# Optimization experiments

Measured on AMD Instinct MI355X. Metric: run time of the kernel, lower is better.

Reference implementation:

```python
import jax, jax.numpy as jnp
import numpy as np


def setup_inputs() -> dict:
    key = jax.random.key(0)
    B, H, C, T = 8, 8, 64, 2048
    qkv = jax.random.normal(key, (B, 3 * H * C, T), dtype=jnp.float32)
    return {"qkv": qkv, "n_heads": H}


def reference(qkv, n_heads):
    # qkv: (B, 3*H*C, T)
    bs, width, length = qkv.shape
    ch = width // (3 * n_heads)
    q, k, v = jnp.split(qkv, 3, axis=1)          # each (B, H*C, T)
    scale = ch ** (-0.25)
    q = (q * scale).reshape(bs * n_heads, ch, length)
    k = (k * scale).reshape(bs * n_heads, ch, length)
    v = v.reshape(bs * n_heads, ch, length)
    # weight[b, t, s] = sum_c q[b,c,t] * k[b,c,s]
    weight = jnp.einsum('bct,bcs->bts', q, k)
    weight = jax.nn.softmax(weight.astype(jnp.float32), axis=-1).astype(qkv.dtype)
    out = jnp.einsum('bts,bcs->bct', weight, v)   # (B*H, C, T)
    return out.reshape(bs, n_heads * ch, length)
```

## Files before the change

### kernel.cpp

```cpp
#include <hip/hip_runtime.h>

typedef __bf16 bf16x4 __attribute__((ext_vector_type(4)));
typedef __bf16 bf16x8 __attribute__((ext_vector_type(8)));
typedef float floatx4 __attribute__((ext_vector_type(4)));
typedef float floatx16 __attribute__((ext_vector_type(16)));
typedef unsigned uintx2 __attribute__((ext_vector_type(2)));

#define T_SEQ 2048
#define TTILE 512
#define STILE 64
#define LOG2E_SCALE 0.18033688011112042f

__device__ __forceinline__ unsigned cvt_pk_bf16(float a, float b) {
    unsigned r;
    asm("v_cvt_pk_bf16_f32 %0, %1, %2" : "=v"(r) : "v"(a), "v"(b));
    return r;
}
__device__ __forceinline__ unsigned short bf16_bits(float a) {
    return (unsigned short)((__builtin_bit_cast(unsigned, a) + 0x8000u) >> 16);
}

__global__ __launch_bounds__(512, 2) void attn_fused(
    const float* __restrict__ qkv, float* __restrict__ out)
{
    __shared__ __align__(16) __bf16 Kt[2][STILE][72];
    __shared__ __align__(16) __bf16 Vs[2][64][72];

    const int tid  = threadIdx.x;
    const int lane = tid & 63;
    const int wave = tid >> 6;
    const int l31  = lane & 31;
    const int g    = lane >> 5;

    const int bh = blockIdx.y;
    const int b = bh >> 3, head = bh & 7;
    const size_t in_base = ((size_t)b * 1536 + head * 64) * T_SEQ;
    const float* Qg = qkv + in_base;
    const float* Kg = qkv + in_base + (size_t)512 * T_SEQ;
    const float* Vg = qkv + in_base + (size_t)1024 * T_SEQ;

    const int tcol0 = blockIdx.x * TTILE + wave * 64 + l31;
    const int tcol1 = tcol0 + 32;

    bf16x8 qf[2][4];
    #pragma unroll
    for (int kb = 0; kb < 4; ++kb)
        #pragma unroll
        for (int j = 0; j < 8; ++j) {
            size_t rowoff = (size_t)(kb * 16 + g * 8 + j) * T_SEQ;
            qf[0][kb][j] = (__bf16)(Qg[rowoff + tcol0] * LOG2E_SCALE);
            qf[1][kb][j] = (__bf16)(Qg[rowoff + tcol1] * LOG2E_SCALE);
        }

    floatx16 zf;
    #pragma unroll
    for (int r = 0; r < 16; ++r) zf[r] = 0.0f;

    union U4 { unsigned u[4]; bf16x8 v; };
    U4 one0, one1;
    {
        unsigned p0 = (l31 == 0) ? 0x3F803F80u : 0u;
        unsigned p1 = (l31 == 1) ? 0x3F803F80u : 0u;
        one0.u[0] = p0; one0.u[1] = p0; one0.u[2] = p0; one0.u[3] = p0;
        one1.u[0] = p1; one1.u[1] = p1; one1.u[2] = p1; one1.u[3] = p1;
    }

    floatx16 Oa[2][2];
    floatx16 La = zf;
    Oa[0][0] = zf; Oa[0][1] = zf; Oa[1][0] = zf; Oa[1][1] = zf;

    int cc[2], ss[2];
    size_t goff[2];
    #pragma unroll
    for (int r = 0; r < 2; ++r) {
        int i = tid + r * 512;
        cc[r] = i >> 4;
        ss[r] = (i & 15) * 4;
        goff[r] = (size_t)cc[r] * T_SEQ + ss[r];
    }
    const int ph = (tid >> 1) & 3;

    floatx4 kr[2], vr[2];
    #pragma unroll
    for (int r = 0; r < 2; ++r) {
        kr[r] = *(const floatx4*)(Kg + goff[r]);
        vr[r] = *(const floatx4*)(Vg + goff[r]);
    }
    #pragma unroll
    for (int r = 0; r < 2; ++r) {
        int c = cc[r], s4 = ss[r];
        #pragma unroll
        for (int k = 0; k < 4; ++k) {
            int d = (k + ph) & 3;
            *(unsigned short*)&Kt[0][s4 + d][c] = bf16_bits(kr[r][d]);
        }
        union { unsigned u[2]; bf16x4 v; } vb;
        vb.u[0] = cvt_pk_bf16(vr[r][0], vr[r][1]);
        vb.u[1] = cvt_pk_bf16(vr[r][2], vr[r][3]);
        *(bf16x4*)&Vs[0][c][s4] = vb.v;
    }

#define QKTSTEP(ROWB, SaT0, SaT1)                                             \
    {                                                                         \
        bf16x8 kf = *(const bf16x8*)&KtR[(ROWB) + l31][g * 8];                \
        SaT0 = __builtin_amdgcn_mfma_f32_32x32x16_bf16(kf, qf[0][0], zf, 0, 0, 0); \
        SaT1 = __builtin_amdgcn_mfma_f32_32x32x16_bf16(kf, qf[1][0], zf, 0, 0, 0); \
    }                                                                         \
    _Pragma("unroll")                                                         \
    for (int kb = 1; kb < 4; ++kb) {                                          \
        bf16x8 kf = *(const bf16x8*)&KtR[(ROWB) + l31][kb * 16 + g * 8];      \
        SaT0 = __builtin_amdgcn_mfma_f32_32x32x16_bf16(kf, qf[0][kb], SaT0, 0, 0, 0); \
        SaT1 = __builtin_amdgcn_mfma_f32_32x32x16_bf16(kf, qf[1][kb], SaT1, 0, 0, 0); \
    }

#define SOFTMAX2(SaT0, SaT1, pf)                                              \
    _Pragma("unroll")                                                         \
    for (int tt = 0; tt < 2; ++tt) {                                          \
        const floatx16& Sa_ = tt ? SaT1 : SaT0;                               \
        float p_[16];                                                         \
        _Pragma("unroll")                                                     \
        for (int r = 0; r < 16; ++r)                                          \
            p_[r] = __builtin_amdgcn_exp2f(Sa_[r]);                           \
        unsigned d_[8];                                                       \
        _Pragma("unroll")                                                     \
        for (int q = 0; q < 8; ++q)                                           \
            d_[q] = cvt_pk_bf16(p_[2 * q], p_[2 * q + 1]);                    \
        _Pragma("unroll")                                                     \
        for (int kb = 0; kb < 2; ++kb) {                                      \
            uintx2 s02 = __builtin_amdgcn_permlane32_swap(                    \
                d_[4 * kb + 0], d_[4 * kb + 2], false, false);                \
            uintx2 s13 = __builtin_amdgcn_permlane32_swap(                    \
                d_[4 * kb + 1], d_[4 * kb + 3], false, false);                \
            U4 fu_;                                                           \
            fu_.u[0] = s02[0]; fu_.u[1] = s13[0];                             \
            fu_.u[2] = s02[1]; fu_.u[3] = s13[1];                             \
            pf[tt][kb] = fu_.v;                                               \
        }                                                                     \
    }

#define PVSTEP(pf, kb2base)                                                   \
    _Pragma("unroll")                                                         \
    for (int mc = 0; mc < 2; ++mc)                                            \
        _Pragma("unroll")                                                     \
        for (int kb = 0; kb < 2; ++kb) {                                      \
            bf16x8 vf = *(const bf16x8*)&VsR[mc * 32 + l31][(kb2base + kb) * 16 + g * 8]; \
            Oa[0][mc] = __builtin_amdgcn_mfma_f32_32x32x16_bf16(vf, pf[0][kb], Oa[0][mc], 0, 0, 0); \
            Oa[1][mc] = __builtin_amdgcn_mfma_f32_32x32x16_bf16(vf, pf[1][kb], Oa[1][mc], 0, 0, 0); \
        }                                                                     \
    _Pragma("unroll")                                                         \
    for (int kb = 0; kb < 2; ++kb) {                                          \
        La = __builtin_amdgcn_mfma_f32_32x32x16_bf16(one0.v, pf[0][kb], La, 0, 0, 0); \
        La = __builtin_amdgcn_mfma_f32_32x32x16_bf16(one1.v, pf[1][kb], La, 0, 0, 0); \
    }

    for (int it = 0; it < T_SEQ / STILE; ++it) {
        const int rb = it & 1;
        const int s_next = (it + 1) * STILE;
        const bool pref = (s_next < T_SEQ);

        __syncthreads();

        if (pref) {
            #pragma unroll
            for (int r = 0; r < 2; ++r) {
                kr[r] = *(const floatx4*)(Kg + goff[r] + s_next);
                vr[r] = *(const floatx4*)(Vg + goff[r] + s_next);
            }
        }

        const __bf16 (*KtR)[72] = Kt[rb];
        const __bf16 (*VsR)[72] = Vs[rb];

        floatx16 Sa00, Sa01;
        QKTSTEP(0, Sa00, Sa01)

        bf16x8 pfA[2][2];
        SOFTMAX2(Sa00, Sa01, pfA)

        floatx16 Sa10, Sa11;
        QKTSTEP(32, Sa10, Sa11)

        PVSTEP(pfA, 0)

        bf16x8 pfB[2][2];
        SOFTMAX2(Sa10, Sa11, pfB)

        PVSTEP(pfB, 2)

        if (pref) {
            __bf16 (*KtW)[72] = Kt[rb ^ 1];
            __bf16 (*VsW)[72] = Vs[rb ^ 1];
            #pragma unroll
            for (int r = 0; r < 2; ++r) {
                int c = cc[r], s4 = ss[r];
                #pragma unroll
                for (int k = 0; k < 4; ++k) {
                    int d = (k + ph) & 3;
                    *(unsigned short*)&KtW[s4 + d][c] = bf16_bits(kr[r][d]);
                }
                union { unsigned u[2]; bf16x4 v; } vb;
                vb.u[0] = cvt_pk_bf16(vr[r][0], vr[r][1]);
                vb.u[1] = cvt_pk_bf16(vr[r][2], vr[r][3]);
                *(bf16x4*)&VsW[c][s4] = vb.v;
            }
        }
    }

    float d0 = La[0], d1 = La[1];
    float rl0 = 1.0f / (d0 + __shfl_xor(d0, 32));
    float rl1 = 1.0f / (d1 + __shfl_xor(d1, 32));

    const size_t out_base = ((size_t)b * 512 + head * 64) * T_SEQ;
    #pragma unroll
    for (int mc = 0; mc < 2; ++mc)
        #pragma unroll
        for (int r = 0; r < 16; ++r) {
            int c = mc * 32 + (r & 3) + 8 * (r >> 2) + 4 * g;
            size_t row = out_base + (size_t)c * T_SEQ;
            out[row + tcol0] = Oa[0][mc][r] * rl0;
            out[row + tcol1] = Oa[1][mc][r] * rl1;
        }
}

extern "C" void kernel_launch(void* const* d_in, const int* in_sizes, int n_in,
                              void* d_out, int out_size, void* d_ws, size_t ws_size,
                              hipStream_t stream) {
    const float* qkv = (const float*)d_in[0];
    float* out = (float*)d_out;
    dim3 grid(T_SEQ / TTILE, 64);
    attn_fused<<<grid, dim3(512), 0, stream>>>(qkv, out);
}
```

Measured before the change: 202.7 us.

## Halve per-wave query tile, raise occupancy, and remap blocks for XCD locality

```diff
diff --git a/kernel.cpp b/kernel.cpp
--- a/kernel.cpp
+++ b/kernel.cpp
@@ -7,7 +7,7 @@
 typedef unsigned uintx2 __attribute__((ext_vector_type(2)));
 
 #define T_SEQ 2048
-#define TTILE 512
+#define TTILE 256
 #define STILE 64
 #define LOG2E_SCALE 0.18033688011112042f
 
@@ -20,7 +20,7 @@
     return (unsigned short)((__builtin_bit_cast(unsigned, a) + 0x8000u) >> 16);
 }
 
-__global__ __launch_bounds__(512, 2) void attn_fused(
+__global__ __launch_bounds__(512, 4) void attn_fused(
     const float* __restrict__ qkv, float* __restrict__ out)
 {
     __shared__ __align__(16) __bf16 Kt[2][STILE][72];
@@ -32,24 +32,27 @@
     const int l31  = lane & 31;
     const int g    = lane >> 5;
 
-    const int bh = blockIdx.y;
+    const int f   = blockIdx.y * 8 + blockIdx.x;
+    const int xcd = f & 7;
+    const int idx = f >> 3;
+    const int bh  = xcd * 8 + (idx >> 3);
+    const int xb  = idx & 7;
+
     const int b = bh >> 3, head = bh & 7;
     const size_t in_base = ((size_t)b * 1536 + head * 64) * T_SEQ;
     const float* Qg = qkv + in_base;
     const float* Kg = qkv + in_base + (size_t)512 * T_SEQ;
     const float* Vg = qkv + in_base + (size_t)1024 * T_SEQ;
 
-    const int tcol0 = blockIdx.x * TTILE + wave * 64 + l31;
-    const int tcol1 = tcol0 + 32;
-
-    bf16x8 qf[2][4];
+    const int tcol = xb * TTILE + wave * 32 + l31;
+
+    bf16x8 qf[4];
     #pragma unroll
     for (int kb = 0; kb < 4; ++kb)
         #pragma unroll
         for (int j = 0; j < 8; ++j) {
             size_t rowoff = (size_t)(kb * 16 + g * 8 + j) * T_SEQ;
-            qf[0][kb][j] = (__bf16)(Qg[rowoff + tcol0] * LOG2E_SCALE);
-            qf[1][kb][j] = (__bf16)(Qg[rowoff + tcol1] * LOG2E_SCALE);
+            qf[kb][j] = (__bf16)(Qg[rowoff + tcol] * LOG2E_SCALE);
         }
 
     floatx16 zf;
@@ -57,17 +60,15 @@
     for (int r = 0; r < 16; ++r) zf[r] = 0.0f;
 
     union U4 { unsigned u[4]; bf16x8 v; };
-    U4 one0, one1;
+    U4 one0;
     {
         unsigned p0 = (l31 == 0) ? 0x3F803F80u : 0u;
-        unsigned p1 = (l31 == 1) ? 0x3F803F80u : 0u;
         one0.u[0] = p0; one0.u[1] = p0; one0.u[2] = p0; one0.u[3] = p0;
-        one1.u[0] = p1; one1.u[1] = p1; one1.u[2] = p1; one1.u[3] = p1;
-    }
-
-    floatx16 Oa[2][2];
+    }
+
+    floatx16 Oa[2];
     floatx16 La = zf;
-    Oa[0][0] = zf; Oa[0][1] = zf; Oa[1][0] = zf; Oa[1][1] = zf;
+    Oa[0] = zf; Oa[1] = zf;
 
     int cc[2], ss[2];
     size_t goff[2];
@@ -100,27 +101,23 @@
         *(bf16x4*)&Vs[0][c][s4] = vb.v;
     }
 
-#define QKTSTEP(ROWB, SaT0, SaT1)                                             \
+#define QKTSTEP(ROWB, Sa)                                                     \
     {                                                                         \
         bf16x8 kf = *(const bf16x8*)&KtR[(ROWB) + l31][g * 8];                \
-        SaT0 = __builtin_amdgcn_mfma_f32_32x32x16_bf16(kf, qf[0][0], zf, 0, 0, 0); \
-        SaT1 = __builtin_amdgcn_mfma_f32_32x32x16_bf16(kf, qf[1][0], zf, 0, 0, 0); \
+        Sa = __builtin_amdgcn_mfma_f32_32x32x16_bf16(kf, qf[0], zf, 0, 0, 0); \
     }                                                                         \
     _Pragma("unroll")                                                         \
     for (int kb = 1; kb < 4; ++kb) {                                          \
         bf16x8 kf = *(const bf16x8*)&KtR[(ROWB) + l31][kb * 16 + g * 8];      \
-        SaT0 = __builtin_amdgcn_mfma_f32_32x32x16_bf16(kf, qf[0][kb], SaT0, 0, 0, 0); \
-        SaT1 = __builtin_amdgcn_mfma_f32_32x32x16_bf16(kf, qf[1][kb], SaT1, 0, 0, 0); \
-    }
-
-#define SOFTMAX2(SaT0, SaT1, pf)                                              \
-    _Pragma("unroll")                                                         \
-    for (int tt = 0; tt < 2; ++tt) {                                          \
-        const floatx16& Sa_ = tt ? SaT1 : SaT0;                               \
+        Sa = __builtin_amdgcn_mfma_f32_32x32x16_bf16(kf, qf[kb], Sa, 0, 0, 0); \
+    }
+
+#define SOFTMAX1(Sa, pf)                                                      \
+    {                                                                         \
         float p_[16];                                                         \
         _Pragma("unroll")                                                     \
         for (int r = 0; r < 16; ++r)                                          \
-            p_[r] = __builtin_amdgcn_exp2f(Sa_[r]);                           \
+            p_[r] = __builtin_amdgcn_exp2f(Sa[r]);                            \
         unsigned d_[8];                                                       \
         _Pragma("unroll")                                                     \
         for (int q = 0; q < 8; ++q)                                           \
@@ -134,7 +131,7 @@
             U4 fu_;                                                           \
             fu_.u[0] = s02[0]; fu_.u[1] = s13[0];                             \
             fu_.u[2] = s02[1]; fu_.u[3] = s13[1];                             \
-            pf[tt][kb] = fu_.v;                                               \
+            pf[kb] = fu_.v;                                                   \
         }                                                                     \
     }
 
@@ -144,14 +141,11 @@
         _Pragma("unroll")                                                     \
         for (int kb = 0; kb < 2; ++kb) {                                      \
             bf16x8 vf = *(const bf16x8*)&VsR[mc * 32 + l31][(kb2base + kb) * 16 + g * 8]; \
-            Oa[0][mc] = __builtin_amdgcn_mfma_f32_32x32x16_bf16(vf, pf[0][kb], Oa[0][mc], 0, 0, 0); \
-            Oa[1][mc] = __builtin_amdgcn_mfma_f32_32x32x16_bf16(vf, pf[1][kb], Oa[1][mc], 0, 0, 0); \
+            Oa[mc] = __builtin_amdgcn_mfma_f32_32x32x16_bf16(vf, pf[kb], Oa[mc], 0, 0, 0); \
         }                                                                     \
     _Pragma("unroll")                                                         \
-    for (int kb = 0; kb < 2; ++kb) {                                          \
-        La = __builtin_amdgcn_mfma_f32_32x32x16_bf16(one0.v, pf[0][kb], La, 0, 0, 0); \
-        La = __builtin_amdgcn_mfma_f32_32x32x16_bf16(one1.v, pf[1][kb], La, 0, 0, 0); \
-    }
+    for (int kb = 0; kb < 2; ++kb)                                            \
+        La = __builtin_amdgcn_mfma_f32_32x32x16_bf16(one0.v, pf[kb], La, 0, 0, 0);
 
     for (int it = 0; it < T_SEQ / STILE; ++it) {
         const int rb = it & 1;
@@ -171,20 +165,17 @@
         const __bf16 (*KtR)[72] = Kt[rb];
         const __bf16 (*VsR)[72] = Vs[rb];
 
-        floatx16 Sa00, Sa01;
-        QKTSTEP(0, Sa00, Sa01)
-
-        bf16x8 pfA[2][2];
-        SOFTMAX2(Sa00, Sa01, pfA)
-
-        floatx16 Sa10, Sa11;
-        QKTSTEP(32, Sa10, Sa11)
-
+        floatx16 Sa0;
+        QKTSTEP(0, Sa0)
+        bf16x8 pfA[2];
+        SOFTMAX1(Sa0, pfA)
+
+        floatx16 Sa1;
+        QKTSTEP(32, Sa1)
         PVSTEP(pfA, 0)
 
-        bf16x8 pfB[2][2];
-        SOFTMAX2(Sa10, Sa11, pfB)
-
+        bf16x8 pfB[2];
+        SOFTMAX1(Sa1, pfB)
         PVSTEP(pfB, 2)
 
         if (pref) {
@@ -206,9 +197,8 @@
         }
     }
 
-    float d0 = La[0], d1 = La[1];
-    float rl0 = 1.0f / (d0 + __shfl_xor(d0, 32));
-    float rl1 = 1.0f / (d1 + __shfl_xor(d1, 32));
+    float d0 = La[0];
+    float rl = 1.0f / (d0 + __shfl_xor(d0, 32));
 
     const size_t out_base = ((size_t)b * 512 + head * 64) * T_SEQ;
     #pragma unroll
@@ -217,8 +207,7 @@
         for (int r = 0; r < 16; ++r) {
             int c = mc * 32 + (r & 3) + 8 * (r >> 2) + 4 * g;
             size_t row = out_base + (size_t)c * T_SEQ;
-            out[row + tcol0] = Oa[0][mc][r] * rl0;
-            out[row + tcol1] = Oa[1][mc][r] * rl1;
+            out[row + tcol] = Oa[mc][r] * rl;
         }
 }
 
```

After: 220.9 us. +9.0%, slower.
